# Kernel optimization log

Measured on AMD Instinct MI355X. Metric: run time of the kernel, lower is better.

Reference implementation:

```python
import jax, jax.numpy as jnp
import numpy as np

N_NODES = 100000
N_EDGES = 1600000
IN_DIM = 256
HID = 32
HEADS = 4
NEG_SLOPE = 0.2


def _seg_softmax(e, seg, n):
    # numerically stable softmax of e [E, H] over segments (destination nodes)
    m = jax.ops.segment_max(e, seg, num_segments=n)
    ex = jnp.exp(e - m[seg])
    s = jax.ops.segment_sum(ex, seg, num_segments=n)
    return ex / (s[seg] + 1e-16)


def _gat_layer(x, W, a_src, a_dst, b, src, dst, n):
    H, D = a_src.shape
    h = (x @ W).reshape(n, H, D)                       # [N, H, D]
    e_src = jnp.sum(h * a_src, axis=-1)                # [N, H]
    e_dst = jnp.sum(h * a_dst, axis=-1)                # [N, H]
    e = jax.nn.leaky_relu(e_src[src] + e_dst[dst], NEG_SLOPE)  # [E, H]
    alpha = _seg_softmax(e, dst, n)                    # [E, H]
    msg = h[src] * alpha[:, :, None]                   # [E, H, D]
    out = jax.ops.segment_sum(msg, dst, num_segments=n)
    return out.reshape(n, H * D) + b


def setup_inputs() -> dict:
    key = jax.random.key(0)
    ks = jax.random.split(key, 20)
    x = jax.random.normal(ks[0], (N_NODES, IN_DIM), dtype=jnp.float32)
    edge_index = jax.random.randint(ks[1], (2, N_EDGES), 0, N_NODES, dtype=jnp.int64)
    s = 0.05
    inp = {"x": x, "edge_index": edge_index}
    inp["W_in"] = jax.random.normal(ks[2], (IN_DIM, HID), dtype=jnp.float32) * s
    inp["b_in"] = jnp.zeros((HID,), dtype=jnp.float32)
    in_dims = [HID, HID * HEADS, HID * HEADS]
    for l in range(3):
        k = jax.random.split(ks[3 + l], 4)
        inp[f"W{l}"] = jax.random.normal(k[0], (in_dims[l], HEADS * HID), dtype=jnp.float32) * s
        inp[f"a_src{l}"] = jax.random.normal(k[1], (HEADS, HID), dtype=jnp.float32) * s
        inp[f"a_dst{l}"] = jax.random.normal(k[2], (HEADS, HID), dtype=jnp.float32) * s
        inp[f"b{l}"] = jnp.zeros((HEADS * HID,), dtype=jnp.float32)
    return inp


def reference(x, edge_index, W_in, b_in,
              W0, a_src0, a_dst0, b0,
              W1, a_src1, a_dst1, b1,
              W2, a_src2, a_dst2, b2):
    n = x.shape[0]
    # PyG GATConv adds self-loops by default
    loops = jnp.arange(n, dtype=edge_index.dtype)
    src = jnp.concatenate([edge_index[0], loops])
    dst = jnp.concatenate([edge_index[1], loops])

    h = jax.nn.relu(x @ W_in + b_in)
    params = [(W0, a_src0, a_dst0, b0), (W1, a_src1, a_dst1, b1), (W2, a_src2, a_dst2, b2)]
    for (W, a_s, a_d, b) in params:
        h = _gat_layer(h, W, a_s, a_d, b, src, dst, n)
        h = jax.nn.elu(h)
        # dropout omitted (eval mode / deterministic reference)
    return h
```

## Files before the change

### kernel.cpp

```cpp
#include <hip/hip_runtime.h>
#include <hip/hip_fp16.h>

#define NN 100000
#define NE 1600000
#define ET (NE + NN)
#define BKW 512
#define NBK ((NN + BKW - 1) / BKW)
#define LCOL_CAP 12288
#define EPB 16384

__device__ __forceinline__ unsigned enc_f32(float v) {
    unsigned b = __float_as_uint(v);
    return b ^ ((b & 0x80000000u) ? 0xFFFFFFFFu : 0x80000000u);
}
__device__ __forceinline__ float dec_f32(unsigned u) {
    unsigned b = (u & 0x80000000u) ? (u ^ 0x80000000u) : ~u;
    return __uint_as_float(b);
}


__global__ __launch_bounds__(256) void lin_relu2(const float* __restrict__ x,
                                                 const float* __restrict__ W,
                                                 const float* __restrict__ b,
                                                 float* __restrict__ h) {
    __shared__ float Wl[256 * 32];
    int t = threadIdx.x;
    for (int j = 0; j < 8; ++j) {
        int f = t + 256 * j;
        *(float4*)&Wl[f * 4] = *(const float4*)(W + f * 4);
    }
    __syncthreads();

    int row = (blockIdx.x * 256 + t) >> 3;
    int c0  = (t & 7) * 4;
    const float* xr = x + (long long)row * 256;
    float4 acc = {0.f, 0.f, 0.f, 0.f};
    for (int k4 = 0; k4 < 64; ++k4) {
        float4 xv = *(const float4*)(xr + k4 * 4);
        float4 w0 = *(const float4*)&Wl[(k4 * 4 + 0) * 32 + c0];
        float4 w1 = *(const float4*)&Wl[(k4 * 4 + 1) * 32 + c0];
        float4 w2 = *(const float4*)&Wl[(k4 * 4 + 2) * 32 + c0];
        float4 w3 = *(const float4*)&Wl[(k4 * 4 + 3) * 32 + c0];
        acc.x += xv.x * w0.x + xv.y * w1.x + xv.z * w2.x + xv.w * w3.x;
        acc.y += xv.x * w0.y + xv.y * w1.y + xv.z * w2.y + xv.w * w3.y;
        acc.z += xv.x * w0.z + xv.y * w1.z + xv.z * w2.z + xv.w * w3.z;
        acc.w += xv.x * w0.w + xv.y * w1.w + xv.z * w2.w + xv.w * w3.w;
    }
    float4 bv = *(const float4*)(b + c0);
    acc.x = fmaxf(acc.x + bv.x, 0.f);
    acc.y = fmaxf(acc.y + bv.y, 0.f);
    acc.z = fmaxf(acc.z + bv.z, 0.f);
    acc.w = fmaxf(acc.w + bv.w, 0.f);
    *(float4*)(h + (long long)row * 32 + c0) = acc;
}

template<int K>
__global__ __launch_bounds__(256) void gemm_att5(const float* __restrict__ hin,
                                                 const float* __restrict__ W,
                                                 const float* __restrict__ asrc,
                                                 const float* __restrict__ adst,
                                                 __half* __restrict__ hph,
                                                 float* __restrict__ es,
                                                 float* __restrict__ ed,
                                                 unsigned* __restrict__ mxl) {
    __shared__ float hl[64][K + 4];
    __shared__ unsigned lmx[8];
    int t = threadIdx.x;
    int base = blockIdx.x * 64;

    if (K == 128) {
        for (int j = 0; j < 8; ++j) {
            int f = t + 256 * j;
            int row = f >> 5;
            int kq = f & 31;
            int gr = base + row;
            float4 v = {0.f, 0.f, 0.f, 0.f};
            if (gr < NN) v = *(const float4*)(hin + (long long)gr * 128 + kq * 4);
            *(float4*)&hl[row][kq * 4] = v;
        }
    } else {
        for (int j = 0; j < 2; ++j) {
            int f = t + 256 * j;
            int row = f >> 3;
            int kq = f & 7;
            int gr = base + row;
            float4 v = {0.f, 0.f, 0.f, 0.f};
            if (gr < NN) v = *(const float4*)(hin + (long long)gr * 32 + kq * 4);
            *(float4*)&hl[row][kq * 4] = v;
        }
    }
    if (t < 8) lmx[t] = 0u;
    __syncthreads();

    int cg = t & 31, c0 = cg * 4;
    int rq = t >> 5, r0 = rq * 8;
    float4 acc[8];
    #pragma unroll
    for (int i = 0; i < 8; ++i) acc[i] = make_float4(0.f, 0.f, 0.f, 0.f);

    for (int k4 = 0; k4 < K / 4; ++k4) {
        float4 w0 = *(const float4*)(W + (k4 * 4 + 0) * 128 + c0);
        float4 w1 = *(const float4*)(W + (k4 * 4 + 1) * 128 + c0);
        float4 w2 = *(const float4*)(W + (k4 * 4 + 2) * 128 + c0);
        float4 w3 = *(const float4*)(W + (k4 * 4 + 3) * 128 + c0);
        #pragma unroll
        for (int i = 0; i < 8; ++i) {
            float4 hv = *(const float4*)&hl[r0 + i][k4 * 4];
            acc[i].x += hv.x * w0.x + hv.y * w1.x + hv.z * w2.x + hv.w * w3.x;
            acc[i].y += hv.x * w0.y + hv.y * w1.y + hv.z * w2.y + hv.w * w3.y;
            acc[i].z += hv.x * w0.z + hv.y * w1.z + hv.z * w2.z + hv.w * w3.z;
            acc[i].w += hv.x * w0.w + hv.y * w1.w + hv.z * w2.w + hv.w * w3.w;
        }
    }

    int head = cg >> 3;
    int d0 = (cg & 7) * 4;
    float4 as4 = *(const float4*)(asrc + head * 32 + d0);
    float4 ad4 = *(const float4*)(adst + head * 32 + d0);
    float smax = -1e30f, dmax = -1e30f;
    #pragma unroll
    for (int i = 0; i < 8; ++i) {
        int gr = base + r0 + i;
        if (gr >= NN) break;
        __half2 p0 = __floats2half2_rn(acc[i].x, acc[i].y);
        __half2 p1 = __floats2half2_rn(acc[i].z, acc[i].w);
        uint2 pk;
        pk.x = *(unsigned*)&p0;
        pk.y = *(unsigned*)&p1;
        *(uint2*)(hph + (long long)gr * 128 + c0) = pk;
        float ps = acc[i].x * as4.x + acc[i].y * as4.y + acc[i].z * as4.z + acc[i].w * as4.w;
        float pd = acc[i].x * ad4.x + acc[i].y * ad4.y + acc[i].z * ad4.z + acc[i].w * ad4.w;
        for (int off = 1; off < 8; off <<= 1) {
            ps += __shfl_xor(ps, off, 8);
            pd += __shfl_xor(pd, off, 8);
        }
        if ((cg & 7) == 0) {
            es[gr * 4 + head] = ps;
            ed[gr * 4 + head] = pd;
            smax = fmaxf(smax, ps);
            dmax = fmaxf(dmax, pd);
        }
    }
    if ((cg & 7) == 0) {
        atomicMax(&lmx[head], enc_f32(smax));
        atomicMax(&lmx[4 + head], enc_f32(dmax));
    }
    __syncthreads();
    if (t < 8) atomicMax(mxl + t, lmx[t]);
}


__global__ __launch_bounds__(256) void bucket_hist(const int* __restrict__ ei,
                                                   int* __restrict__ bhist) {
    __shared__ int lh[NBK];
    int t = threadIdx.x;
    for (int i = t; i < NBK; i += 256) lh[i] = 0;
    __syncthreads();
    for (long long e = (long long)blockIdx.x * 256 + t; e < ET; e += (long long)gridDim.x * 256) {
        int dst = (e < NE) ? ei[NE + e] : (int)(e - NE);
        atomicAdd(&lh[dst >> 9], 1);
    }
    __syncthreads();
    for (int i = t; i < NBK; i += 256) if (lh[i]) atomicAdd(&bhist[i], lh[i]);
}

__global__ __launch_bounds__(256) void bucket_scan(const int* __restrict__ bhist,
                                                   int* __restrict__ bbase,
                                                   int* __restrict__ bcur) {
    __shared__ int ls[256];
    int t = threadIdx.x;
    int v = (t < NBK) ? bhist[t] : 0;
    ls[t] = v;
    __syncthreads();
    for (int off = 1; off < 256; off <<= 1) {
        int u = (t >= off) ? ls[t - off] : 0;
        __syncthreads();
        ls[t] += u;
        __syncthreads();
    }
    if (t < NBK) { int b0 = ls[t] - v; bbase[t] = b0; bcur[t] = b0; }
    if (t == 0) bbase[NBK] = ET;
}

__global__ __launch_bounds__(256) void bucket_scatter(const int* __restrict__ ei,
                                                      int* __restrict__ bcur,
                                                      unsigned* __restrict__ brec) {
    __shared__ int lcnt[NBK];
    __shared__ int lbase[NBK];
    int t = threadIdx.x;
    long long e0 = (long long)blockIdx.x * EPB;
    for (int i = t; i < NBK; i += 256) lcnt[i] = 0;
    __syncthreads();
    for (int j = 0; j < EPB / 256; ++j) {
        long long e = e0 + j * 256 + t;
        if (e < ET) {
            int dst = (e < NE) ? ei[NE + e] : (int)(e - NE);
            atomicAdd(&lcnt[dst >> 9], 1);
        }
    }
    __syncthreads();
    for (int i = t; i < NBK; i += 256) {
        int c = lcnt[i];
        lbase[i] = c ? atomicAdd(&bcur[i], c) : 0;
        lcnt[i] = 0;
    }
    __syncthreads();
    for (int j = 0; j < EPB / 256; ++j) {
        long long e = e0 + j * 256 + t;
        if (e < ET) {
            int src, dst;
            if (e < NE) { src = ei[e]; dst = ei[NE + e]; }
            else        { src = dst = (int)(e - NE); }
            int b = dst >> 9;
            int off = atomicAdd(&lcnt[b], 1);
            brec[lbase[b] + off] = ((unsigned)(dst & 511) << 17) | (unsigned)src;
        }
    }
}

__global__ __launch_bounds__(256) void bucket_csr(const unsigned* __restrict__ brec,
                                                  const int* __restrict__ bbase,
                                                  int* __restrict__ row_ptr,
                                                  int* __restrict__ col) {
    __shared__ int ldeg[BKW];
    __shared__ int lrp[BKW + 1];
    __shared__ int lcur[BKW];
    __shared__ int ls[256];
    __shared__ int lcol[LCOL_CAP];
    int t = threadIdx.x, b = blockIdx.x;
    int rbeg = bbase[b], rend = bbase[b + 1];
    int cnt = rend - rbeg;
    for (int i = t; i < BKW; i += 256) ldeg[i] = 0;
    __syncthreads();
    for (int i = t; i < cnt; i += 256) {
        unsigned r = brec[rbeg + i];
        atomicAdd(&ldeg[r >> 17], 1);
    }
    __syncthreads();
    int a0 = ldeg[2 * t], a1 = ldeg[2 * t + 1];
    int pl = a0 + a1;
    ls[t] = pl;
    __syncthreads();
    for (int off = 1; off < 256; off <<= 1) {
        int u = (t >= off) ? ls[t - off] : 0;
        __syncthreads();
        ls[t] += u;
        __syncthreads();
    }
    int eb = ls[t] - pl;
    lrp[2 * t] = eb;
    lrp[2 * t + 1] = eb + a0;
    lcur[2 * t] = eb;
    lcur[2 * t + 1] = eb + a0;
    if (t == 255) lrp[BKW] = ls[255];
    __syncthreads();
    int gn0 = b * BKW;
    int nnb = min(BKW, NN - gn0);
    for (int i = t; i <= nnb; i += 256) row_ptr[gn0 + i] = rbeg + lrp[i];
    for (int i = t; i < cnt; i += 256) {
        unsigned r = brec[rbeg + i];
        int pos = atomicAdd(&lcur[r >> 17], 1);
        lcol[pos] = (int)(r & 0x1FFFFu);
    }
    __syncthreads();
    for (int i = t; i < cnt; i += 256) col[rbeg + i] = lcol[i];
}

__global__ __launch_bounds__(256) void gat_aggregate3(
        const int* __restrict__ row_ptr, const int* __restrict__ col,
        const float* __restrict__ es, const float* __restrict__ ed,
        const unsigned* __restrict__ mx, const __half* __restrict__ hph,
        const float* __restrict__ b, float* __restrict__ out) {
    int tid = blockIdx.x * 256 + threadIdx.x;
    int n = tid >> 4;
    int t = tid & 15;
    if (n >= NN) return;
    int head = t >> 2;
    int beg = row_ptr[n], end = row_ptr[n + 1];

    float Craw = dec_f32(mx[head]) + dec_f32(mx[4 + head]);
    float C = Craw > 0.f ? Craw : 0.2f * Craw;
    float edv = ed[n * 4 + head];

    float acc[8] = {0.f, 0.f, 0.f, 0.f, 0.f, 0.f, 0.f, 0.f};
    float ws = 0.f;
    const __half* hb = hph + (long long)t * 8;

    int i = beg;
    for (; i + 3 < end; i += 4) {
        int s0 = col[i], s1 = col[i + 1], s2 = col[i + 2], s3 = col[i + 3];
        float l0 = es[s0 * 4 + head] + edv;
        float l1 = es[s1 * 4 + head] + edv;
        float l2 = es[s2 * 4 + head] + edv;
        float l3 = es[s3 * 4 + head] + edv;
        uint4 g0 = *(const uint4*)(hb + (long long)s0 * 128);
        uint4 g1 = *(const uint4*)(hb + (long long)s1 * 128);
        uint4 g2 = *(const uint4*)(hb + (long long)s2 * 128);
        uint4 g3 = *(const uint4*)(hb + (long long)s3 * 128);
        l0 = l0 > 0.f ? l0 : 0.2f * l0;
        l1 = l1 > 0.f ? l1 : 0.2f * l1;
        l2 = l2 > 0.f ? l2 : 0.2f * l2;
        l3 = l3 > 0.f ? l3 : 0.2f * l3;
        float w0 = __expf(l0 - C);
        float w1 = __expf(l1 - C);
        float w2 = __expf(l2 - C);
        float w3 = __expf(l3 - C);
        ws += (w0 + w1) + (w2 + w3);
        float2 f;
        f = __half22float2(*(__half2*)&g0.x); acc[0] += w0 * f.x; acc[1] += w0 * f.y;
        f = __half22float2(*(__half2*)&g0.y); acc[2] += w0 * f.x; acc[3] += w0 * f.y;
        f = __half22float2(*(__half2*)&g0.z); acc[4] += w0 * f.x; acc[5] += w0 * f.y;
        f = __half22float2(*(__half2*)&g0.w); acc[6] += w0 * f.x; acc[7] += w0 * f.y;
        f = __half22float2(*(__half2*)&g1.x); acc[0] += w1 * f.x; acc[1] += w1 * f.y;
        f = __half22float2(*(__half2*)&g1.y); acc[2] += w1 * f.x; acc[3] += w1 * f.y;
        f = __half22float2(*(__half2*)&g1.z); acc[4] += w1 * f.x; acc[5] += w1 * f.y;
        f = __half22float2(*(__half2*)&g1.w); acc[6] += w1 * f.x; acc[7] += w1 * f.y;
        f = __half22float2(*(__half2*)&g2.x); acc[0] += w2 * f.x; acc[1] += w2 * f.y;
        f = __half22float2(*(__half2*)&g2.y); acc[2] += w2 * f.x; acc[3] += w2 * f.y;
        f = __half22float2(*(__half2*)&g2.z); acc[4] += w2 * f.x; acc[5] += w2 * f.y;
        f = __half22float2(*(__half2*)&g2.w); acc[6] += w2 * f.x; acc[7] += w2 * f.y;
        f = __half22float2(*(__half2*)&g3.x); acc[0] += w3 * f.x; acc[1] += w3 * f.y;
        f = __half22float2(*(__half2*)&g3.y); acc[2] += w3 * f.x; acc[3] += w3 * f.y;
        f = __half22float2(*(__half2*)&g3.z); acc[4] += w3 * f.x; acc[5] += w3 * f.y;
        f = __half22float2(*(__half2*)&g3.w); acc[6] += w3 * f.x; acc[7] += w3 * f.y;
    }
    for (; i < end; ++i) {
        int s = col[i];
        float lv = es[s * 4 + head] + edv;
        lv = lv > 0.f ? lv : 0.2f * lv;
        float w = __expf(lv - C);
        ws += w;
        uint4 g = *(const uint4*)(hb + (long long)s * 128);
        float2 f;
        f = __half22float2(*(__half2*)&g.x); acc[0] += w * f.x; acc[1] += w * f.y;
        f = __half22float2(*(__half2*)&g.y); acc[2] += w * f.x; acc[3] += w * f.y;
        f = __half22float2(*(__half2*)&g.z); acc[4] += w * f.x; acc[5] += w * f.y;
        f = __half22float2(*(__half2*)&g.w); acc[6] += w * f.x; acc[7] += w * f.y;
    }
    float sv = ws + 1e-16f;
    float4 b0 = *(const float4*)(b + t * 8);
    float4 b1 = *(const float4*)(b + t * 8 + 4);
    float4 v0, v1;
    v0.x = acc[0] / sv + b0.x; v0.y = acc[1] / sv + b0.y;
    v0.z = acc[2] / sv + b0.z; v0.w = acc[3] / sv + b0.w;
    v1.x = acc[4] / sv + b1.x; v1.y = acc[5] / sv + b1.y;
    v1.z = acc[6] / sv + b1.z; v1.w = acc[7] / sv + b1.w;
    v0.x = v0.x > 0.f ? v0.x : expm1f(v0.x);
    v0.y = v0.y > 0.f ? v0.y : expm1f(v0.y);
    v0.z = v0.z > 0.f ? v0.z : expm1f(v0.z);
    v0.w = v0.w > 0.f ? v0.w : expm1f(v0.w);
    v1.x = v1.x > 0.f ? v1.x : expm1f(v1.x);
    v1.y = v1.y > 0.f ? v1.y : expm1f(v1.y);
    v1.z = v1.z > 0.f ? v1.z : expm1f(v1.z);
    v1.w = v1.w > 0.f ? v1.w : expm1f(v1.w);
    *(float4*)(out + (long long)n * 128 + t * 8) = v0;
    *(float4*)(out + (long long)n * 128 + t * 8 + 4) = v1;
}


extern "C" void kernel_launch(void* const* d_in, const int* in_sizes, int n_in,
                              void* d_out, int out_size, void* d_ws, size_t ws_size,
                              hipStream_t stream) {
    const float* x    = (const float*)d_in[0];
    const int*   ei   = (const int*)d_in[1];
    const float* W_in = (const float*)d_in[2];
    const float* b_in = (const float*)d_in[3];
    const float* W[3]  = {(const float*)d_in[4], (const float*)d_in[8],  (const float*)d_in[12]};
    const float* As[3] = {(const float*)d_in[5], (const float*)d_in[9],  (const float*)d_in[13]};
    const float* Ad[3] = {(const float*)d_in[6], (const float*)d_in[10], (const float*)d_in[14]};
    const float* Bs[3] = {(const float*)d_in[7], (const float*)d_in[11], (const float*)d_in[15]};

    float*  h0     = (float*)d_ws;
    __half* hph    = (__half*)(h0 + (size_t)NN * 32);
    float*  es     = (float*)(hph + (size_t)NN * 128);
    float*  ed     = es + (size_t)NN * 4;
    int*    row_ptr= (int*)(ed + (size_t)NN * 4);
    int*    bhist  = row_ptr + (NN + 1);
    int*    bbase  = bhist + NBK;
    int*    bcur   = bbase + (NBK + 1);
    unsigned* mx   = (unsigned*)(bcur + NBK);
    unsigned* brec = (unsigned*)(mx + 24);
    int*    colb   = (int*)(brec + ET);
    float*  accb   = (float*)d_out;

    hipMemsetAsync(bhist, 0, NBK * sizeof(int), stream);
    hipMemsetAsync(mx, 0, 24 * sizeof(unsigned), stream);
    bucket_hist<<<512, 256, 0, stream>>>(ei, bhist);
    bucket_scan<<<1, 256, 0, stream>>>(bhist, bbase, bcur);
    bucket_scatter<<<(ET + EPB - 1) / EPB, 256, 0, stream>>>(ei, bcur, brec);
    bucket_csr<<<NBK, 256, 0, stream>>>(brec, bbase, row_ptr, colb);

    lin_relu2<<<3125, 256, 0, stream>>>(x, W_in, b_in, h0);

    const float* in = h0;
    for (int l = 0; l < 3; ++l) {
        if (l == 0)
            gemm_att5<32><<<1563, 256, 0, stream>>>(in, W[0], As[0], Ad[0], hph, es, ed, mx);
        else
            gemm_att5<128><<<1563, 256, 0, stream>>>(in, W[l], As[l], Ad[l], hph, es, ed, mx + l * 8);
        gat_aggregate3<<<6250, 256, 0, stream>>>(row_ptr, colb, es, ed, mx + l * 8, hph, Bs[l], accb);
        in = accb;
    }
}
```

Before: 556.2 us.

## Use fp16 MFMA GEMM for layers 1-2 with half-precision intermediate activations

Replaces the scalar fp32 shared-memory GEMM for the 128-wide GAT layers with an MFMA 16x16x32 f16 kernel. Weights are pre-swizzled into fragment layout by a small prep kernel. The aggregation kernel now writes fp16 activations for intermediate layers, which halves their traffic and feeds the MFMA kernel directly. This trades precision in the hidden activations for fewer bytes moved and higher GEMM throughput, and the epilogue's scattered 2-byte hph stores may be poorly coalesced.

```diff
diff --git a/kernel.cpp b/kernel.cpp
--- a/kernel.cpp
+++ b/kernel.cpp
@@ -8,6 +8,9 @@
 #define NBK ((NN + BKW - 1) / BKW)
 #define LCOL_CAP 12288
 #define EPB 16384
+
+typedef _Float16 half8_t __attribute__((ext_vector_type(8)));
+typedef float f32x4_t __attribute__((ext_vector_type(4)));
 
 __device__ __forceinline__ unsigned enc_f32(float v) {
     unsigned b = __float_as_uint(v);
@@ -68,26 +71,14 @@
     int t = threadIdx.x;
     int base = blockIdx.x * 64;
 
-    if (K == 128) {
-        for (int j = 0; j < 8; ++j) {
-            int f = t + 256 * j;
-            int row = f >> 5;
-            int kq = f & 31;
-            int gr = base + row;
-            float4 v = {0.f, 0.f, 0.f, 0.f};
-            if (gr < NN) v = *(const float4*)(hin + (long long)gr * 128 + kq * 4);
-            *(float4*)&hl[row][kq * 4] = v;
-        }
-    } else {
-        for (int j = 0; j < 2; ++j) {
-            int f = t + 256 * j;
-            int row = f >> 3;
-            int kq = f & 7;
-            int gr = base + row;
-            float4 v = {0.f, 0.f, 0.f, 0.f};
-            if (gr < NN) v = *(const float4*)(hin + (long long)gr * 32 + kq * 4);
-            *(float4*)&hl[row][kq * 4] = v;
-        }
+    for (int j = 0; j < K / 16; ++j) {
+        int f = t + 256 * j;
+        int row = f / (K / 4);
+        int kq = f % (K / 4);
+        int gr = base + row;
+        float4 v = {0.f, 0.f, 0.f, 0.f};
+        if (gr < NN) v = *(const float4*)(hin + (long long)gr * K + kq * 4);
+        *(float4*)&hl[row][kq * 4] = v;
     }
     if (t < 8) lmx[t] = 0u;
     __syncthreads();
@@ -149,6 +140,119 @@
     if (t < 8) atomicMax(mxl + t, lmx[t]);
 }
 
+__global__ __launch_bounds__(256) void wf_prep(const float* __restrict__ W,
+                                               _Float16* __restrict__ Wf) {
+    int id = blockIdx.x * 256 + threadIdx.x;
+    if (id >= 2048) return;
+    int lane = id & 63;
+    int q = id >> 6;
+    int ks = q & 3;
+    int n = q >> 2;
+    int col = n * 16 + (lane & 15);
+    int k0 = ks * 32 + ((lane >> 4) << 3);
+    _Float16 tmp[8];
+    #pragma unroll
+    for (int j = 0; j < 8; ++j) tmp[j] = (_Float16)W[(k0 + j) * 128 + col];
+    *(half8_t*)(Wf + (size_t)id * 8) = *(half8_t*)tmp;
+}
+
+__global__ __launch_bounds__(256) void gemm_mfma(const __half* __restrict__ ah,
+                                                 const _Float16* __restrict__ Wf,
+                                                 const float* __restrict__ asrc,
+                                                 const float* __restrict__ adst,
+                                                 __half* __restrict__ hph,
+                                                 float* __restrict__ es,
+                                                 float* __restrict__ ed,
+                                                 unsigned* __restrict__ mxl) {
+    __shared__ unsigned lmx[8];
+    int t = threadIdx.x;
+    if (t < 8) lmx[t] = 0u;
+    __syncthreads();
+
+    int lane = t & 63, wid = t >> 6;
+    int li = lane & 15, lg = lane >> 4;
+    int base = blockIdx.x * 128 + wid * 32;
+    int r0 = base + li, r1 = r0 + 16;
+    long long r0c = min(r0, NN - 1), r1c = min(r1, NN - 1);
+    const _Float16* A = (const _Float16*)ah;
+
+    f32x4_t acc[2][8];
+    #pragma unroll
+    for (int m = 0; m < 2; ++m)
+        #pragma unroll
+        for (int n = 0; n < 8; ++n) acc[m][n] = (f32x4_t){0.f, 0.f, 0.f, 0.f};
+
+    #pragma unroll
+    for (int ks = 0; ks < 4; ++ks) {
+        half8_t a0 = *(const half8_t*)(A + r0c * 128 + ks * 32 + lg * 8);
+        half8_t a1 = *(const half8_t*)(A + r1c * 128 + ks * 32 + lg * 8);
+        #pragma unroll
+        for (int n = 0; n < 8; ++n) {
+            half8_t b = *(const half8_t*)(Wf + (size_t)((n * 4 + ks) * 64 + lane) * 8);
+            acc[0][n] = __builtin_amdgcn_mfma_f32_16x16x32_f16(a0, b, acc[0][n], 0, 0, 0);
+            acc[1][n] = __builtin_amdgcn_mfma_f32_16x16x32_f16(a1, b, acc[1][n], 0, 0, 0);
+        }
+    }
+
+    float as_lo[4], as_hi[4], ad_lo[4], ad_hi[4];
+    #pragma unroll
+    for (int h = 0; h < 4; ++h) {
+        as_lo[h] = asrc[h * 32 + li];
+        as_hi[h] = asrc[h * 32 + 16 + li];
+        ad_lo[h] = adst[h * 32 + li];
+        ad_hi[h] = adst[h * 32 + 16 + li];
+    }
+
+    float smax[4] = {-1e30f, -1e30f, -1e30f, -1e30f};
+    float dmax[4] = {-1e30f, -1e30f, -1e30f, -1e30f};
+    #pragma unroll
+    for (int m = 0; m < 2; ++m) {
+        #pragma unroll
+        for (int r = 0; r < 4; ++r) {
+            int gr = base + m * 16 + lg * 4 + r;
+            bool valid = gr < NN;
+            float ps[4], pd[4];
+            #pragma unroll
+            for (int h = 0; h < 4; ++h) {
+                float va = acc[m][2 * h][r];
+                float vb = acc[m][2 * h + 1][r];
+                if (valid) {
+                    hph[(long long)gr * 128 + h * 32 + li] = __float2half(va);
+                    hph[(long long)gr * 128 + h * 32 + 16 + li] = __float2half(vb);
+                }
+                ps[h] = va * as_lo[h] + vb * as_hi[h];
+                pd[h] = va * ad_lo[h] + vb * ad_hi[h];
+            }
+            #pragma unroll
+            for (int off = 1; off < 16; off <<= 1) {
+                #pragma unroll
+                for (int h = 0; h < 4; ++h) {
+                    ps[h] += __shfl_xor(ps[h], off);
+                    pd[h] += __shfl_xor(pd[h], off);
+                }
+            }
+            if (li == 0 && valid) {
+                #pragma unroll
+                for (int h = 0; h < 4; ++h) {
+                    es[gr * 4 + h] = ps[h];
+                    ed[gr * 4 + h] = pd[h];
+                    smax[h] = fmaxf(smax[h], ps[h]);
+                    dmax[h] = fmaxf(dmax[h], pd[h]);
+                }
+            }
+        }
+    }
+    if (li == 0) {
+        #pragma unroll
+        for (int h = 0; h < 4; ++h) {
+            atomicMax(&lmx[h], enc_f32(smax[h]));
+            atomicMax(&lmx[4 + h], enc_f32(dmax[h]));
+        }
+    }
+    __syncthreads();
+    if (t < 8) atomicMax(mxl + t, lmx[t]);
+}
+
 
 __global__ __launch_bounds__(256) void bucket_hist(const int* __restrict__ ei,
                                                    int* __restrict__ bhist) {
@@ -266,11 +370,12 @@
     for (int i = t; i < cnt; i += 256) col[rbeg + i] = lcol[i];
 }
 
-__global__ __launch_bounds__(256) void gat_aggregate3(
+__global__ __launch_bounds__(256) void gat_aggregate4(
         const int* __restrict__ row_ptr, const int* __restrict__ col,
         const float* __restrict__ es, const float* __restrict__ ed,
         const unsigned* __restrict__ mx, const __half* __restrict__ hph,
-        const float* __restrict__ b, float* __restrict__ out) {
+        const float* __restrict__ b, float* __restrict__ outf,
+        __half* __restrict__ outh) {
     int tid = blockIdx.x * 256 + threadIdx.x;
     int n = tid >> 4;
     int t = tid & 15;
@@ -338,23 +443,23 @@
         f = __half22float2(*(__half2*)&g.w); acc[6] += w * f.x; acc[7] += w * f.y;
     }
     float sv = ws + 1e-16f;
-    float4 b0 = *(const float4*)(b + t * 8);
-    float4 b1 = *(const float4*)(b + t * 8 + 4);
-    float4 v0, v1;
-    v0.x = acc[0] / sv + b0.x; v0.y = acc[1] / sv + b0.y;
-    v0.z = acc[2] / sv + b0.z; v0.w = acc[3] / sv + b0.w;
-    v1.x = acc[4] / sv + b1.x; v1.y = acc[5] / sv + b1.y;
-    v1.z = acc[6] / sv + b1.z; v1.w = acc[7] / sv + b1.w;
-    v0.x = v0.x > 0.f ? v0.x : expm1f(v0.x);
-    v0.y = v0.y > 0.f ? v0.y : expm1f(v0.y);
-    v0.z = v0.z > 0.f ? v0.z : expm1f(v0.z);
-    v0.w = v0.w > 0.f ? v0.w : expm1f(v0.w);
-    v1.x = v1.x > 0.f ? v1.x : expm1f(v1.x);
-    v1.y = v1.y > 0.f ? v1.y : expm1f(v1.y);
-    v1.z = v1.z > 0.f ? v1.z : expm1f(v1.z);
-    v1.w = v1.w > 0.f ? v1.w : expm1f(v1.w);
-    *(float4*)(out + (long long)n * 128 + t * 8) = v0;
-    *(float4*)(out + (long long)n * 128 + t * 8 + 4) = v1;
+    float vals[8];
+    #pragma unroll
+    for (int j = 0; j < 8; ++j) {
+        float v = acc[j] / sv + b[t * 8 + j];
+        vals[j] = v > 0.f ? v : expm1f(v);
+    }
+    if (outf) {
+        float4 v0 = {vals[0], vals[1], vals[2], vals[3]};
+        float4 v1 = {vals[4], vals[5], vals[6], vals[7]};
+        *(float4*)(outf + (long long)n * 128 + t * 8) = v0;
+        *(float4*)(outf + (long long)n * 128 + t * 8 + 4) = v1;
+    } else {
+        __half o[8];
+        #pragma unroll
+        for (int j = 0; j < 8; ++j) o[j] = __float2half(vals[j]);
+        *(uint4*)(outh + (long long)n * 128 + t * 8) = *(uint4*)o;
+    }
 }
 
 
@@ -370,18 +475,20 @@
     const float* Ad[3] = {(const float*)d_in[6], (const float*)d_in[10], (const float*)d_in[14]};
     const float* Bs[3] = {(const float*)d_in[7], (const float*)d_in[11], (const float*)d_in[15]};
 
-    float*  h0     = (float*)d_ws;
-    __half* hph    = (__half*)(h0 + (size_t)NN * 32);
-    float*  es     = (float*)(hph + (size_t)NN * 128);
-    float*  ed     = es + (size_t)NN * 4;
-    int*    row_ptr= (int*)(ed + (size_t)NN * 4);
+    float*    h0   = (float*)d_ws;
+    __half*   hph  = (__half*)(h0 + (size_t)NN * 32);
+    __half*   ah   = hph + (size_t)NN * 128;
+    float*    es   = (float*)(ah + (size_t)NN * 128);
+    float*    ed   = es + (size_t)NN * 4;
+    int*   row_ptr = (int*)(ed + (size_t)NN * 4);
     int*    bhist  = row_ptr + (NN + 1);
     int*    bbase  = bhist + NBK;
     int*    bcur   = bbase + (NBK + 1);
     unsigned* mx   = (unsigned*)(bcur + NBK);
-    unsigned* brec = (unsigned*)(mx + 24);
+    _Float16* Wf1  = (_Float16*)(mx + 24);
+    _Float16* Wf2  = Wf1 + 2048 * 8;
+    unsigned* brec = (unsigned*)(Wf2 + 2048 * 8);
     int*    colb   = (int*)(brec + ET);
-    float*  accb   = (float*)d_out;
 
     hipMemsetAsync(bhist, 0, NBK * sizeof(int), stream);
     hipMemsetAsync(mx, 0, 24 * sizeof(unsigned), stream);
@@ -391,14 +498,16 @@
     bucket_csr<<<NBK, 256, 0, stream>>>(brec, bbase, row_ptr, colb);
 
     lin_relu2<<<3125, 256, 0, stream>>>(x, W_in, b_in, h0);
-
-    const float* in = h0;
-    for (int l = 0; l < 3; ++l) {
-        if (l == 0)
-            gemm_att5<32><<<1563, 256, 0, stream>>>(in, W[0], As[0], Ad[0], hph, es, ed, mx);
-        else
-            gemm_att5<128><<<1563, 256, 0, stream>>>(in, W[l], As[l], Ad[l], hph, es, ed, mx + l * 8);
-        gat_aggregate3<<<6250, 256, 0, stream>>>(row_ptr, colb, es, ed, mx + l * 8, hph, Bs[l], accb);
-        in = accb;
-    }
-}
+    wf_prep<<<8, 256, 0, stream>>>(W[1], Wf1);
+    wf_prep<<<8, 256, 0, stream>>>(W[2], Wf2);
+
+    gemm_att5<32><<<1563, 256, 0, stream>>>(h0, W[0], As[0], Ad[0], hph, es, ed, mx);
+    gat_aggregate4<<<6250, 256, 0, stream>>>(row_ptr, colb, es, ed, mx, hph, Bs[0],
+                                             nullptr, ah);
+    gemm_mfma<<<782, 256, 0, stream>>>(ah, Wf1, As[1], Ad[1], hph, es, ed, mx + 8);
+    gat_aggregate4<<<6250, 256, 0, stream>>>(row_ptr, colb, es, ed, mx + 8, hph, Bs[1],
+                                             nullptr, ah);
+    gemm_mfma<<<782, 256, 0, stream>>>(ah, Wf2, As[2], Ad[2], hph, es, ed, mx + 16);
+    gat_aggregate4<<<6250, 256, 0, stream>>>(row_ptr, colb, es, ed, mx + 16, hph, Bs[2],
+                                             (float*)d_out, nullptr);
+}
```

After: 499.3 us. 1.11x faster.
